# Performance work log

Measured on AMD Instinct MI355X. Metric: run time of the kernel, lower is better.

## Reference

```python
import jax, jax.numpy as jnp
import numpy as np

B, N, X, Y, W1, W2 = 2, 6, 8, 8, 8, 8
DIM, HEADS, DHEAD = 128, 4, 32
HD = HEADS * DHEAD
EPS = 1e-5


def setup_inputs() -> dict:
    key = jax.random.key(0)
    ks = jax.random.split(key, 12)
    d = {}
    d['q'] = jax.random.normal(ks[0], (B, N, X, Y, W1, W2, DIM), jnp.float32)
    d['k'] = jax.random.normal(ks[1], (B, N, X, Y, W1, W2, DIM), jnp.float32)
    d['v'] = jax.random.normal(ks[2], (B, N, X, Y, W1, W2, DIM), jnp.float32)
    d['skip'] = jax.random.normal(ks[3], (B, X, Y, W1, W2, DIM), jnp.float32)
    d['head_gate'] = jax.random.uniform(ks[4], (HEADS,), jnp.float32, 0.5, 1.5)
    # LayerNorm affine params (slightly perturbed so grads are nontrivial)
    d['ln_q_w'] = 1.0 + 0.1 * jax.random.normal(ks[5], (DIM,), jnp.float32)
    d['ln_q_b'] = jnp.zeros((DIM,), jnp.float32)
    d['ln_k_w'] = 1.0 + 0.1 * jax.random.normal(ks[6], (DIM,), jnp.float32)
    d['ln_k_b'] = jnp.zeros((DIM,), jnp.float32)
    d['ln_v_w'] = 1.0 + 0.1 * jax.random.normal(ks[7], (DIM,), jnp.float32)
    d['ln_v_b'] = jnp.zeros((DIM,), jnp.float32)
    # Linear weights, stored as (in, out) so x @ w + b
    s = 0.02
    d['wq'] = s * jax.random.normal(ks[8], (DIM, HD), jnp.float32)
    d['bq'] = jnp.zeros((HD,), jnp.float32)
    d['wk'] = s * jax.random.normal(ks[9], (DIM, HD), jnp.float32)
    d['bk'] = jnp.zeros((HD,), jnp.float32)
    d['wv'] = s * jax.random.normal(ks[10], (DIM, HD), jnp.float32)
    d['bv'] = jnp.zeros((HD,), jnp.float32)
    d['wp'] = s * jax.random.normal(ks[11], (HD, DIM), jnp.float32)
    d['bp'] = jnp.zeros((DIM,), jnp.float32)
    return d


def _ln(x, w, b):
    mu = jnp.mean(x, axis=-1, keepdims=True)
    var = jnp.mean(jnp.square(x - mu), axis=-1, keepdims=True)
    return (x - mu) * jax.lax.rsqrt(var + EPS) * w + b


def _windows(t):
    # (b, n, x, y, w1, w2, d) -> (b, x*y, n*w1*w2, d)
    b, n, x, y, w1, w2, dd = t.shape
    return t.transpose(0, 2, 3, 1, 4, 5, 6).reshape(b, x * y, n * w1 * w2, dd)


def _heads(t):
    # (b, l, t, HEADS*DHEAD) -> (b, m, l, t, DHEAD)
    b, l, tt, _ = t.shape
    return t.reshape(b, l, tt, HEADS, DHEAD).transpose(0, 3, 1, 2, 4)


def reference(q, k, v, skip, head_gate,
              ln_q_w, ln_q_b, ln_k_w, ln_k_b, ln_v_w, ln_v_b,
              wq, bq, wk, bk, wv, bv, wp, bp):
    b, n, x, y, w1, w2, _ = q.shape
    scale = DHEAD ** -0.5
    qh = _heads(_ln(_windows(q), ln_q_w, ln_q_b) @ wq + bq) * scale
    kh = _heads(_ln(_windows(k), ln_k_w, ln_k_b) @ wk + bk)
    vh = _heads(_ln(_windows(v), ln_v_w, ln_v_b) @ wv + bv)
    # per-window attention: l = x*y windows, Q = K = n*w1*w2 tokens
    dot = jnp.einsum('bmlqd,bmlkd->bmlqk', qh, kh)
    dot = dot * head_gate[None, :, None, None, None]
    att = jax.nn.softmax(dot, axis=-1)
    a = jnp.einsum('bmlqk,bmlkd->bmlqd', att, vh)
    a = a.transpose(0, 2, 3, 1, 4).reshape(b, x * y, n * w1 * w2, HD)
    out = a.reshape(b, x, y, n, w1, w2, HD).transpose(0, 3, 1, 2, 4, 5, 6)
    z = out @ wp + bp          # (b, n, x, y, w1, w2, dim)
    z = jnp.mean(z, axis=1)    # mean over agents n
    return z + skip
```

## Files before the change

### kernel.cpp

```cpp
#include <hip/hip_runtime.h>
#include <hip/hip_bf16.h>
#include <cstddef>

#define NB     2
#define NA     6
#define NWIN   64
#define NTOK   384
#define DIM    128
#define NHEADS 4
#define DHEAD  32

typedef __attribute__((ext_vector_type(8))) short short8;
typedef __attribute__((ext_vector_type(4))) float f32x4;

__device__ __forceinline__ unsigned short f2bf(float f) {
    __hip_bfloat16 h = __float2bfloat16(f);
    return *reinterpret_cast<unsigned short*>(&h);
}
__device__ __forceinline__ float bf2f(unsigned short u) {
    union { unsigned int i; float f; } x; x.i = ((unsigned int)u) << 16; return x.f;
}

__global__ __launch_bounds__(256) void wprep_kernel(
    const float* __restrict__ wq, const float* __restrict__ wk,
    const float* __restrict__ wv,
    const float* __restrict__ lnqw, const float* __restrict__ lnkw,
    const float* __restrict__ lnvw,
    const float* __restrict__ lnqb, const float* __restrict__ lnkb,
    const float* __restrict__ lnvb,
    const float* __restrict__ bq, const float* __restrict__ bk,
    const float* __restrict__ bv, const float* __restrict__ gate,
    unsigned short* __restrict__ wt,
    float* __restrict__ scol, float* __restrict__ tcol)
{
    const int bid = blockIdx.x;
    if (bid < 192) {
        const int e = bid * 256 + threadIdx.x;
        const int mat = e >> 14, i = e & 16383;
        const int kk = i >> 7, c = i & 127;
        const float* src = (mat == 0) ? wq : (mat == 1) ? wk : wv;
        const float* lnw = (mat == 0) ? lnqw : (mat == 1) ? lnkw : lnvw;
        const float s = (mat == 0) ? (0.17677669529663687f * gate[c >> 5]) : 1.0f;
        wt[(mat << 14) + c * DIM + kk] = f2bf(src[i] * lnw[kk] * s);
        return;
    }
    const int mat = bid - 192;
    const int c = threadIdx.x;
    if (c >= DIM) return;
    const float* src  = (mat == 0) ? wq : (mat == 1) ? wk : wv;
    const float* lnw  = (mat == 0) ? lnqw : (mat == 1) ? lnkw : lnvw;
    const float* lnb  = (mat == 0) ? lnqb : (mat == 1) ? lnkb : lnvb;
    const float* bias = (mat == 0) ? bq : (mat == 1) ? bk : bv;
    float sa[8] = {0.f,0.f,0.f,0.f,0.f,0.f,0.f,0.f};
    float ta[8] = {0.f,0.f,0.f,0.f,0.f,0.f,0.f,0.f};
#pragma unroll
    for (int k0 = 0; k0 < DIM; k0 += 8) {
        float w0 = src[(k0+0)*DIM+c], w1 = src[(k0+1)*DIM+c];
        float w2 = src[(k0+2)*DIM+c], w3 = src[(k0+3)*DIM+c];
        float w4 = src[(k0+4)*DIM+c], w5 = src[(k0+5)*DIM+c];
        float w6 = src[(k0+6)*DIM+c], w7 = src[(k0+7)*DIM+c];
        sa[0] += lnw[k0+0]*w0; ta[0] += lnb[k0+0]*w0;
        sa[1] += lnw[k0+1]*w1; ta[1] += lnb[k0+1]*w1;
        sa[2] += lnw[k0+2]*w2; ta[2] += lnb[k0+2]*w2;
        sa[3] += lnw[k0+3]*w3; ta[3] += lnb[k0+3]*w3;
        sa[4] += lnw[k0+4]*w4; ta[4] += lnb[k0+4]*w4;
        sa[5] += lnw[k0+5]*w5; ta[5] += lnb[k0+5]*w5;
        sa[6] += lnw[k0+6]*w6; ta[6] += lnb[k0+6]*w6;
        sa[7] += lnw[k0+7]*w7; ta[7] += lnb[k0+7]*w7;
    }
    const float s = ((sa[0]+sa[1])+(sa[2]+sa[3]))+((sa[4]+sa[5])+(sa[6]+sa[7]));
    const float t = ((ta[0]+ta[1])+(ta[2]+ta[3]))+((ta[4]+ta[5])+(ta[6]+ta[7]));
    const float qs = (mat == 0) ? (0.17677669529663687f * gate[c >> 5]) : 1.0f;
    scol[mat * DIM + c] = s * qs;
    tcol[mat * DIM + c] = (t + bias[c]) * qs;
}

#define ACC8(p, q) do { \
    s  += ((p.x + p.y) + (p.z + p.w)) + ((q.x + q.y) + (q.z + q.w)); \
    s2 += ((p.x*p.x + p.y*p.y) + (p.z*p.z + p.w*p.w)) \
        + ((q.x*q.x + q.y*q.y) + (q.z*q.z + q.w*q.w)); } while (0)
#define CVT8(p, q) ({ short8 o_; \
    o_[0]=(short)f2bf(p.x); o_[1]=(short)f2bf(p.y); o_[2]=(short)f2bf(p.z); o_[3]=(short)f2bf(p.w); \
    o_[4]=(short)f2bf(q.x); o_[5]=(short)f2bf(q.y); o_[6]=(short)f2bf(q.z); o_[7]=(short)f2bf(q.w); o_; })

__global__ __launch_bounds__(384) void proj_kernel(
    const float* __restrict__ qx, const float* __restrict__ kx,
    const float* __restrict__ vx,
    const unsigned short* __restrict__ wt,
    const float* __restrict__ scol, const float* __restrict__ tcol,
    unsigned short* __restrict__ qh, unsigned short* __restrict__ kh,
    unsigned short* __restrict__ vh)
{
    __shared__ unsigned short Wl[DIM * DIM];

    const int bid  = blockIdx.x;
    const int mode = bid >> 8;
    const int rr   = bid & 255;
    const int b = rr >> 7, l = (rr >> 1) & 63, ng = rr & 1;

    const float* xin = (mode == 0) ? qx : (mode == 1) ? kx : vx;
    const unsigned short* wtm = wt + (mode << 14);
    const float* sc = scol + mode * DIM;
    const float* tc = tcol + mode * DIM;
    unsigned short* outp = (mode == 0) ? qh : (mode == 1) ? kh : vh;

    const int wv_ = threadIdx.x / 64;
    const int lane = threadIdx.x & 63;
    const int g = lane >> 4, qc = lane & 15;
    const int n  = ng * 3 + (wv_ >> 1);
    const int t0 = (wv_ & 1) * 32;

    short8 wbuf0 = {0,0,0,0,0,0,0,0}, wbuf1 = wbuf0, wbuf2 = wbuf0,
           wbuf3 = wbuf0, wbuf4 = wbuf0, wbuf5 = wbuf0;
    {
        const int e0 = threadIdx.x;
        wbuf0 = *(const short8*)&wtm[(e0 +    0) * 8];
        wbuf1 = *(const short8*)&wtm[(e0 +  384) * 8];
        wbuf2 = *(const short8*)&wtm[(e0 +  768) * 8];
        wbuf3 = *(const short8*)&wtm[(e0 + 1152) * 8];
        wbuf4 = *(const short8*)&wtm[(e0 + 1536) * 8];
        if (e0 + 1920 < 2048) wbuf5 = *(const short8*)&wtm[(e0 + 1920) * 8];
    }

    const float* xp0 = xin + ((size_t)((b * NA + n) * NWIN + l) * 64 + t0 + qc) * DIM + 8 * g;
    const float* xp1 = xp0 + 16 * DIM;
    const float4 u0 = *(const float4*)(xp0 + 0);
    const float4 u1 = *(const float4*)(xp0 + 4);
    const float4 u2 = *(const float4*)(xp0 + 32);
    const float4 u3 = *(const float4*)(xp0 + 36);
    const float4 u4 = *(const float4*)(xp0 + 64);
    const float4 u5 = *(const float4*)(xp0 + 68);
    const float4 u6 = *(const float4*)(xp0 + 96);
    const float4 u7 = *(const float4*)(xp0 + 100);
    const float4 y0 = *(const float4*)(xp1 + 0);
    const float4 y1 = *(const float4*)(xp1 + 4);
    const float4 y2 = *(const float4*)(xp1 + 32);
    const float4 y3 = *(const float4*)(xp1 + 36);
    const float4 y4 = *(const float4*)(xp1 + 64);
    const float4 y5 = *(const float4*)(xp1 + 68);
    const float4 y6 = *(const float4*)(xp1 + 96);
    const float4 y7 = *(const float4*)(xp1 + 100);

    {
        const int e0 = threadIdx.x;
#define WSTORE(eo, bufv) do { const int e_ = e0 + eo; \
        const int col_ = e_ >> 4, k8_ = (e_ & 15) * 8; \
        *(short8*)&Wl[col_ * DIM + (k8_ ^ ((col_ & 7) << 3))] = bufv; } while (0)
        WSTORE(0, wbuf0); WSTORE(384, wbuf1); WSTORE(768, wbuf2);
        WSTORE(1152, wbuf3); WSTORE(1536, wbuf4);
        if (e0 + 1920 < 2048) WSTORE(1920, wbuf5);
#undef WSTORE
    }

    float mu0, rs0, mu1, rs1;
    {
        float s = 0.f, s2 = 0.f;
        ACC8(u0, u1); ACC8(u2, u3); ACC8(u4, u5); ACC8(u6, u7);
        s  += __shfl_xor(s, 16);  s  += __shfl_xor(s, 32);
        s2 += __shfl_xor(s2, 16); s2 += __shfl_xor(s2, 32);
        mu0 = s * (1.0f / 128.0f);
        rs0 = rsqrtf(s2 * (1.0f / 128.0f) - mu0 * mu0 + 1e-5f);
    }
    {
        float s = 0.f, s2 = 0.f;
        ACC8(y0, y1); ACC8(y2, y3); ACC8(y4, y5); ACC8(y6, y7);
        s  += __shfl_xor(s, 16);  s  += __shfl_xor(s, 32);
        s2 += __shfl_xor(s2, 16); s2 += __shfl_xor(s2, 32);
        mu1 = s * (1.0f / 128.0f);
        rs1 = rsqrtf(s2 * (1.0f / 128.0f) - mu1 * mu1 + 1e-5f);
    }

    short8 af0[4], af1[4];
    af0[0] = CVT8(u0, u1); af0[1] = CVT8(u2, u3);
    af0[2] = CVT8(u4, u5); af0[3] = CVT8(u6, u7);
    af1[0] = CVT8(y0, y1); af1[1] = CVT8(y2, y3);
    af1[2] = CVT8(y4, y5); af1[3] = CVT8(y6, y7);
    __syncthreads();

    float m0[4], r0[4], m1[4], r1[4];
    if (mode == 2) {
#pragma unroll
        for (int r = 0; r < 4; ++r) {
            m0[r] = __shfl(mu0, 4 * g + r); r0[r] = __shfl(rs0, 4 * g + r);
            m1[r] = __shfl(mu1, 4 * g + r); r1[r] = __shfl(rs1, 4 * g + r);
        }
    }

    const f32x4 z = {0.f, 0.f, 0.f, 0.f};
    const int swz = (qc & 7) << 3;

#pragma unroll
    for (int ct = 0; ct < 8; ++ct) {
        const int col = ct * 16 + qc;
        short8 wf[4];
#pragma unroll
        for (int c = 0; c < 4; ++c)
            wf[c] = *(const short8*)&Wl[col * DIM + ((c * 32 + 8 * g) ^ swz)];

        f32x4 a0 = z, a1 = z;
        if (mode == 2) {
#pragma unroll
            for (int c = 0; c < 4; ++c) {
                a0 = __builtin_amdgcn_mfma_f32_16x16x32_bf16(af0[c], wf[c], a0, 0, 0, 0);
                a1 = __builtin_amdgcn_mfma_f32_16x16x32_bf16(af1[c], wf[c], a1, 0, 0, 0);
            }
            const float s_c = sc[col], t_c = tc[col];
            const int head = ct >> 1;
            const int d = (ct & 1) * 16 + qc;
            const size_t rowb = ((size_t)(b * NHEADS + head) * NWIN + l) * DHEAD + d;
            unsigned short* dst = outp + rowb * NTOK + n * 64 + t0 + 4 * g;
            ushort4 o;
            o.x = f2bf(r0[0] * (a0[0] - m0[0] * s_c) + t_c);
            o.y = f2bf(r0[1] * (a0[1] - m0[1] * s_c) + t_c);
            o.z = f2bf(r0[2] * (a0[2] - m0[2] * s_c) + t_c);
            o.w = f2bf(r0[3] * (a0[3] - m0[3] * s_c) + t_c);
            *(ushort4*)&dst[0] = o;
            o.x = f2bf(r1[0] * (a1[0] - m1[0] * s_c) + t_c);
            o.y = f2bf(r1[1] * (a1[1] - m1[1] * s_c) + t_c);
            o.z = f2bf(r1[2] * (a1[2] - m1[2] * s_c) + t_c);
            o.w = f2bf(r1[3] * (a1[3] - m1[3] * s_c) + t_c);
            *(ushort4*)&dst[16] = o;
        } else {
#pragma unroll
            for (int c = 0; c < 4; ++c) {
                a0 = __builtin_amdgcn_mfma_f32_16x16x32_bf16(wf[c], af0[c], a0, 0, 0, 0);
                a1 = __builtin_amdgcn_mfma_f32_16x16x32_bf16(wf[c], af1[c], a1, 0, 0, 0);
            }
            const int head = ct >> 1;
            const int d0 = (ct & 1) * 16 + 4 * g;
            const float4 s4 = *(const float4*)&sc[ct * 16 + 4 * g];
            const float4 t4 = *(const float4*)&tc[ct * 16 + 4 * g];
            const size_t hb = (size_t)(b * NHEADS + head) * NWIN + l;
            unsigned short* dst = outp + (hb * NTOK + n * 64 + t0 + qc) * DHEAD + d0;
            ushort4 o;
            o.x = f2bf(rs0 * (a0[0] - mu0 * s4.x) + t4.x);
            o.y = f2bf(rs0 * (a0[1] - mu0 * s4.y) + t4.y);
            o.z = f2bf(rs0 * (a0[2] - mu0 * s4.z) + t4.z);
            o.w = f2bf(rs0 * (a0[3] - mu0 * s4.w) + t4.w);
            *(ushort4*)&dst[0] = o;
            o.x = f2bf(rs1 * (a1[0] - mu1 * s4.x) + t4.x);
            o.y = f2bf(rs1 * (a1[1] - mu1 * s4.y) + t4.y);
            o.z = f2bf(rs1 * (a1[2] - mu1 * s4.z) + t4.z);
            o.w = f2bf(rs1 * (a1[3] - mu1 * s4.w) + t4.w);
            *(ushort4*)&dst[16 * DHEAD] = o;
        }
    }
}

__global__ __launch_bounds__(256) void attn_kernel(
    const unsigned short* __restrict__ qh, const unsigned short* __restrict__ kh,
    const unsigned short* __restrict__ vt, unsigned short* __restrict__ aout)
{
    __shared__ unsigned short P[4][3][16][40];

    const int tid  = threadIdx.x;
    const int w    = tid >> 6;
    const int lane = tid & 63;
    const int g    = lane >> 4;
    const int qc   = lane & 15;

    const int raw = blockIdx.x;
    const int p    = (raw >> 4) * 8 + (raw & 7);
    const int half = (raw >> 3) & 1;
    const int b = p >> 8, h = (p >> 6) & 3, l = p & 63;
    const size_t base = (size_t)((b * NHEADS + h) * NWIN + l) * (NTOK * DHEAD);
    const unsigned short* Qp = qh + base;
    const unsigned short* Kp = kh + base;
    const unsigned short* Vp = vt + base;

    short8 qf[3];
#pragma unroll
    for (int j = 0; j < 3; ++j)
        qf[j] = *(const short8*)(Qp + (size_t)(((half * 4 + w) * 3 + j) * 16 + qc) * DHEAD + 8 * g);

    f32x4 o0[3], o1[3];
    float psum[3];
    const f32x4 z = {0.f, 0.f, 0.f, 0.f};
#pragma unroll
    for (int j = 0; j < 3; ++j) { o0[j] = z; o1[j] = z; psum[j] = 0.f; }

    for (int kc = 0; kc < 12; ++kc) {
        const int k0 = kc * 32;
        const short8 ka0 = *(const short8*)(Kp + (size_t)(k0 + qc) * DHEAD + 8 * g);
        const short8 ka1 = *(const short8*)(Kp + (size_t)(k0 + 16 + qc) * DHEAD + 8 * g);
        const short8 vb0 = *(const short8*)(Vp + (size_t)qc * NTOK + k0 + 8 * g);
        const short8 vb1 = *(const short8*)(Vp + (size_t)(16 + qc) * NTOK + k0 + 8 * g);

#pragma unroll
        for (int j = 0; j < 3; ++j) {
            f32x4 s0 = __builtin_amdgcn_mfma_f32_16x16x32_bf16(ka0, qf[j], z, 0, 0, 0);
            f32x4 s1 = __builtin_amdgcn_mfma_f32_16x16x32_bf16(ka1, qf[j], z, 0, 0, 0);
            const float e0 = __expf(s0[0]), e1 = __expf(s0[1]), e2 = __expf(s0[2]), e3 = __expf(s0[3]);
            const float e4 = __expf(s1[0]), e5 = __expf(s1[1]), e6 = __expf(s1[2]), e7 = __expf(s1[3]);
            psum[j] += ((e0 + e1) + (e2 + e3)) + ((e4 + e5) + (e6 + e7));
            ushort4 pw0, pw1;
            pw0.x = f2bf(e0); pw0.y = f2bf(e1); pw0.z = f2bf(e2); pw0.w = f2bf(e3);
            pw1.x = f2bf(e4); pw1.y = f2bf(e5); pw1.z = f2bf(e6); pw1.w = f2bf(e7);
            *(ushort4*)&P[w][j][qc][4 * g]      = pw0;
            *(ushort4*)&P[w][j][qc][16 + 4 * g] = pw1;
        }
#pragma unroll
        for (int j = 0; j < 3; ++j) {
            const short8 pa = *(const short8*)&P[w][j][qc][8 * g];
            o0[j] = __builtin_amdgcn_mfma_f32_16x16x32_bf16(pa, vb0, o0[j], 0, 0, 0);
            o1[j] = __builtin_amdgcn_mfma_f32_16x16x32_bf16(pa, vb1, o1[j], 0, 0, 0);
        }
    }

#pragma unroll
    for (int j = 0; j < 3; ++j) {
        float ps = psum[j];
        ps += __shfl_xor(ps, 16);
        ps += __shfl_xor(ps, 32);
        const float inv = 1.0f / ps;
        const int q0 = ((half * 4 + w) * 3 + j) * 16;
        const size_t ob = ((size_t)(b * NWIN + l) * NTOK + q0) * (NHEADS * DHEAD) + h * DHEAD + qc;
#pragma unroll
        for (int r = 0; r < 4; ++r) {
            const float iv = __shfl(inv, 4 * g + r);
            aout[ob + (size_t)(4 * g + r) * (NHEADS * DHEAD)]      = f2bf(o0[j][r] * iv);
            aout[ob + (size_t)(4 * g + r) * (NHEADS * DHEAD) + 16] = f2bf(o1[j][r] * iv);
        }
    }
}

__global__ __launch_bounds__(256) void outproj_kernel(
    const unsigned short* __restrict__ a, const float* __restrict__ wp,
    const float* __restrict__ bp, const float* __restrict__ skip,
    float* __restrict__ outp)
{
    __shared__ float at[DIM * 68];
    __shared__ float wl[DIM * 64];

    const int tid = threadIdx.x;
    const int bid = blockIdx.x;
    const int b = bid >> 7, l = (bid >> 1) & 63, cg = bid & 1;
    const int c0 = cg * 64;

#pragma unroll
    for (int rep = 0; rep < 8; ++rep) {
        const int idx = rep * 256 + tid;
        const int row = idx >> 4, cc4 = idx & 15;
        *(float4*)&wl[row * 64 + cc4 * 4] = *(const float4*)&wp[row * 128 + c0 + cc4 * 4];
    }

    const size_t abase = (size_t)(b * NWIN + l) * NTOK * DIM;
#pragma unroll
    for (int r = 0; r < 32; ++r) {
        const int f = tid + 256 * r;
        const int w_ = f >> 7, d = f & 127;
        float s = 0.f;
#pragma unroll
        for (int n = 0; n < NA; ++n)
            s += bf2f(a[abase + (size_t)(n * 64 + w_) * DIM + d]);
        at[d * 68 + w_] = s * (1.0f / 6.0f);
    }
    __syncthreads();

    const int cx = tid & 15, ty = tid >> 4;
    float acc[4][4];
#pragma unroll
    for (int i = 0; i < 4; ++i)
#pragma unroll
        for (int j = 0; j < 4; ++j) acc[i][j] = 0.f;

#pragma unroll 4
    for (int i = 0; i < DIM; ++i) {
        const float4 wa = *(const float4*)&wl[i * 64 + 4 * cx];
        const float4 aa = *(const float4*)&at[i * 68 + 4 * ty];
        acc[0][0] += aa.x * wa.x; acc[0][1] += aa.x * wa.y; acc[0][2] += aa.x * wa.z; acc[0][3] += aa.x * wa.w;
        acc[1][0] += aa.y * wa.x; acc[1][1] += aa.y * wa.y; acc[1][2] += aa.y * wa.z; acc[1][3] += aa.y * wa.w;
        acc[2][0] += aa.z * wa.x; acc[2][1] += aa.z * wa.y; acc[2][2] += aa.z * wa.z; acc[2][3] += aa.z * wa.w;
        acc[3][0] += aa.w * wa.x; acc[3][1] += aa.w * wa.y; acc[3][2] += aa.w * wa.z; acc[3][3] += aa.w * wa.w;
    }

    const float4 bb = *(const float4*)&bp[c0 + 4 * cx];
#pragma unroll
    for (int u = 0; u < 4; ++u) {
        const int w_ = 4 * ty + u;
        const size_t oidx = ((size_t)(b * NWIN + l) * 64 + w_) * DIM + c0 + 4 * cx;
        const float4 sk = *(const float4*)&skip[oidx];
        float4 o;
        o.x = acc[u][0] + bb.x + sk.x;
        o.y = acc[u][1] + bb.y + sk.y;
        o.z = acc[u][2] + bb.z + sk.z;
        o.w = acc[u][3] + bb.w + sk.w;
        *(float4*)&outp[oidx] = o;
    }
}

extern "C" void kernel_launch(void* const* d_in, const int* in_sizes, int n_in,
                              void* d_out, int out_size, void* d_ws, size_t ws_size,
                              hipStream_t stream) {
    const float* q      = (const float*)d_in[0];
    const float* k      = (const float*)d_in[1];
    const float* v      = (const float*)d_in[2];
    const float* skip   = (const float*)d_in[3];
    const float* gate   = (const float*)d_in[4];
    const float* ln_q_w = (const float*)d_in[5];
    const float* ln_q_b = (const float*)d_in[6];
    const float* ln_k_w = (const float*)d_in[7];
    const float* ln_k_b = (const float*)d_in[8];
    const float* ln_v_w = (const float*)d_in[9];
    const float* ln_v_b = (const float*)d_in[10];
    const float* wq     = (const float*)d_in[11];
    const float* bq     = (const float*)d_in[12];
    const float* wk     = (const float*)d_in[13];
    const float* bk     = (const float*)d_in[14];
    const float* wv     = (const float*)d_in[15];
    const float* bv     = (const float*)d_in[16];
    const float* wp     = (const float*)d_in[17];
    const float* bp     = (const float*)d_in[18];
    float* outp = (float*)d_out;

    const size_t per = (size_t)NB * NHEADS * NWIN * NTOK * DHEAD;
    unsigned short* qh = (unsigned short*)d_ws;
    unsigned short* kh = qh + per;
    unsigned short* vh = kh + per;
    unsigned short* wt = vh + per;
    unsigned short* a  = wt + 3 * 16384;
    float* scol = (float*)(a + per);
    float* tcol = scol + 3 * DIM;

    wprep_kernel<<<195, 256, 0, stream>>>(wq, wk, wv, ln_q_w, ln_k_w, ln_v_w,
                                          ln_q_b, ln_k_b, ln_v_b, bq, bk, bv,
                                          gate, wt, scol, tcol);
    proj_kernel<<<768, 384, 0, stream>>>(q, k, v, wt, scol, tcol, qh, kh, vh);
    attn_kernel<<<NB * NHEADS * NWIN * 2, 256, 0, stream>>>(qh, kh, vh, a);
    outproj_kernel<<<NB * NWIN * 2, 256, 0, stream>>>(a, wp, bp, skip, outp);
}
```

Before: 70.51 us.

## Load projection weights via global_load_lds, shrink proj blocks, fold log2e into Q

New measurement: 74.88 us. 6.2% more time.

```diff
diff --git a/kernel.cpp b/kernel.cpp
--- a/kernel.cpp
+++ b/kernel.cpp
@@ -20,6 +20,8 @@
 __device__ __forceinline__ float bf2f(unsigned short u) {
     union { unsigned int i; float f; } x; x.i = ((unsigned int)u) << 16; return x.f;
 }
+
+#define QSCALE (0.17677669529663687f * 1.4426950408889634f)
 
 __global__ __launch_bounds__(256) void wprep_kernel(
     const float* __restrict__ wq, const float* __restrict__ wk,
@@ -40,7 +42,7 @@
         const int kk = i >> 7, c = i & 127;
         const float* src = (mat == 0) ? wq : (mat == 1) ? wk : wv;
         const float* lnw = (mat == 0) ? lnqw : (mat == 1) ? lnkw : lnvw;
-        const float s = (mat == 0) ? (0.17677669529663687f * gate[c >> 5]) : 1.0f;
+        const float s = (mat == 0) ? (QSCALE * gate[c >> 5]) : 1.0f;
         wt[(mat << 14) + c * DIM + kk] = f2bf(src[i] * lnw[kk] * s);
         return;
     }
@@ -70,7 +72,7 @@
     }
     const float s = ((sa[0]+sa[1])+(sa[2]+sa[3]))+((sa[4]+sa[5])+(sa[6]+sa[7]));
     const float t = ((ta[0]+ta[1])+(ta[2]+ta[3]))+((ta[4]+ta[5])+(ta[6]+ta[7]));
-    const float qs = (mat == 0) ? (0.17677669529663687f * gate[c >> 5]) : 1.0f;
+    const float qs = (mat == 0) ? (QSCALE * gate[c >> 5]) : 1.0f;
     scol[mat * DIM + c] = s * qs;
     tcol[mat * DIM + c] = (t + bias[c]) * qs;
 }
@@ -83,7 +85,12 @@
     o_[0]=(short)f2bf(p.x); o_[1]=(short)f2bf(p.y); o_[2]=(short)f2bf(p.z); o_[3]=(short)f2bf(p.w); \
     o_[4]=(short)f2bf(q.x); o_[5]=(short)f2bf(q.y); o_[6]=(short)f2bf(q.z); o_[7]=(short)f2bf(q.w); o_; })
 
-__global__ __launch_bounds__(384) void proj_kernel(
+#define GLOAD_LDS16(gsrc, ldst) \
+    __builtin_amdgcn_global_load_lds( \
+        (const __attribute__((address_space(1))) void*)(gsrc), \
+        (__attribute__((address_space(3))) void*)(ldst), 16, 0, 0)
+
+__global__ __launch_bounds__(256) void proj_kernel(
     const float* __restrict__ qx, const float* __restrict__ kx,
     const float* __restrict__ vx,
     const unsigned short* __restrict__ wt,
@@ -94,9 +101,12 @@
     __shared__ unsigned short Wl[DIM * DIM];
 
     const int bid  = blockIdx.x;
-    const int mode = bid >> 8;
-    const int rr   = bid & 255;
-    const int b = rr >> 7, l = (rr >> 1) & 63, ng = rr & 1;
+    const int mode = bid / 384;
+    const int rr   = bid - mode * 384;
+    const int b = rr / 192;
+    const int rr2 = rr - b * 192;
+    const int l = rr2 / 3;
+    const int ng = rr2 - l * 3;
 
     const float* xin = (mode == 0) ? qx : (mode == 1) ? kx : vx;
     const unsigned short* wtm = wt + (mode << 14);
@@ -104,22 +114,19 @@
     const float* tc = tcol + mode * DIM;
     unsigned short* outp = (mode == 0) ? qh : (mode == 1) ? kh : vh;
 
-    const int wv_ = threadIdx.x / 64;
+    const int wv_ = threadIdx.x >> 6;
     const int lane = threadIdx.x & 63;
     const int g = lane >> 4, qc = lane & 15;
-    const int n  = ng * 3 + (wv_ >> 1);
+    const int n  = ng * 2 + (wv_ >> 1);
     const int t0 = (wv_ & 1) * 32;
 
-    short8 wbuf0 = {0,0,0,0,0,0,0,0}, wbuf1 = wbuf0, wbuf2 = wbuf0,
-           wbuf3 = wbuf0, wbuf4 = wbuf0, wbuf5 = wbuf0;
-    {
-        const int e0 = threadIdx.x;
-        wbuf0 = *(const short8*)&wtm[(e0 +    0) * 8];
-        wbuf1 = *(const short8*)&wtm[(e0 +  384) * 8];
-        wbuf2 = *(const short8*)&wtm[(e0 +  768) * 8];
-        wbuf3 = *(const short8*)&wtm[(e0 + 1152) * 8];
-        wbuf4 = *(const short8*)&wtm[(e0 + 1536) * 8];
-        if (e0 + 1920 < 2048) wbuf5 = *(const short8*)&wtm[(e0 + 1920) * 8];
+#pragma unroll
+    for (int i = 0; i < 8; ++i) {
+        const int cbase = (wv_ * 8 + i) * 64;
+        const int cidx = cbase + lane;
+        const int col = cidx >> 4, j = cidx & 15;
+        const unsigned short* src = wtm + col * DIM + ((j ^ (col & 7)) << 3);
+        GLOAD_LDS16(src, Wl + cbase * 8);
     }
 
     const float* xp0 = xin + ((size_t)((b * NA + n) * NWIN + l) * 64 + t0 + qc) * DIM + 8 * g;
@@ -140,17 +147,6 @@
     const float4 y5 = *(const float4*)(xp1 + 68);
     const float4 y6 = *(const float4*)(xp1 + 96);
     const float4 y7 = *(const float4*)(xp1 + 100);
-
-    {
-        const int e0 = threadIdx.x;
-#define WSTORE(eo, bufv) do { const int e_ = e0 + eo; \
-        const int col_ = e_ >> 4, k8_ = (e_ & 15) * 8; \
-        *(short8*)&Wl[col_ * DIM + (k8_ ^ ((col_ & 7) << 3))] = bufv; } while (0)
-        WSTORE(0, wbuf0); WSTORE(384, wbuf1); WSTORE(768, wbuf2);
-        WSTORE(1152, wbuf3); WSTORE(1536, wbuf4);
-        if (e0 + 1920 < 2048) WSTORE(1920, wbuf5);
-#undef WSTORE
-    }
 
     float mu0, rs0, mu1, rs1;
     {
@@ -290,8 +286,8 @@
         for (int j = 0; j < 3; ++j) {
             f32x4 s0 = __builtin_amdgcn_mfma_f32_16x16x32_bf16(ka0, qf[j], z, 0, 0, 0);
             f32x4 s1 = __builtin_amdgcn_mfma_f32_16x16x32_bf16(ka1, qf[j], z, 0, 0, 0);
-            const float e0 = __expf(s0[0]), e1 = __expf(s0[1]), e2 = __expf(s0[2]), e3 = __expf(s0[3]);
-            const float e4 = __expf(s1[0]), e5 = __expf(s1[1]), e6 = __expf(s1[2]), e7 = __expf(s1[3]);
+            const float e0 = exp2f(s0[0]), e1 = exp2f(s0[1]), e2 = exp2f(s0[2]), e3 = exp2f(s0[3]);
+            const float e4 = exp2f(s1[0]), e5 = exp2f(s1[1]), e6 = exp2f(s1[2]), e7 = exp2f(s1[3]);
             psum[j] += ((e0 + e1) + (e2 + e3)) + ((e4 + e5) + (e6 + e7));
             ushort4 pw0, pw1;
             pw0.x = f2bf(e0); pw0.y = f2bf(e1); pw0.z = f2bf(e2); pw0.w = f2bf(e3);
@@ -425,7 +421,7 @@
     wprep_kernel<<<195, 256, 0, stream>>>(wq, wk, wv, ln_q_w, ln_k_w, ln_v_w,
                                           ln_q_b, ln_k_b, ln_v_b, bq, bk, bv,
                                           gate, wt, scol, tcol);
-    proj_kernel<<<768, 384, 0, stream>>>(q, k, v, wt, scol, tcol, qh, kh, vh);
+    proj_kernel<<<1152, 256, 0, stream>>>(q, k, v, wt, scol, tcol, qh, kh, vh);
     attn_kernel<<<NB * NHEADS * NWIN * 2, 256, 0, stream>>>(qh, kh, vh, a);
     outproj_kernel<<<NB * NWIN * 2, 256, 0, stream>>>(a, wp, bp, skip, outp);
 }
```
